# Optimization experiments

Measured on AMD Instinct MI355X. Metric: run time of the kernel, lower is better.

## Reference

```python
import jax, jax.numpy as jnp
import numpy as np

B, T, N = 32, 64, 2048
HID, HEADS, DH, BOT, MAX_LAG = 256, 8, 32, 64, 7


def setup_inputs() -> dict:
    key = jax.random.key(0)
    ks = jax.random.split(key, 12)
    def nrm(k, shape, s=0.05):
        return jax.random.normal(k, shape, jnp.float32) * s
    # delay logits init as in the module: log(softmaxed exp decay)
    w = np.exp(-np.arange(MAX_LAG + 1) / 3.0)
    w = w / w.sum()
    delay_logits = jnp.asarray(np.log(w + 1e-8), jnp.float32)
    # row-normalized adjacency prior (done in __init__ of the module)
    adj_raw = jax.random.uniform(ks[0], (N, N), jnp.float32)
    adj_prior = adj_raw / (adj_raw.sum(-1, keepdims=True) + 1e-8)
    return {
        "x": jax.random.normal(ks[1], (B, T, N), jnp.float32),
        "features": jax.random.normal(ks[2], (B, N, HID), jnp.float32),
        "delay_logits": delay_logits,
        "w_dp": nrm(ks[3], (1, HID)), "b_dp": jnp.zeros((HID,), jnp.float32),
        "w_qkv_low": nrm(ks[4], (HID, 3 * BOT)), "b_qkv_low": jnp.zeros((3 * BOT,), jnp.float32),
        "w_qkv_high": nrm(ks[5], (3 * BOT, 3 * HID)), "b_qkv_high": jnp.zeros((3 * HID,), jnp.float32),
        "w_out_low": nrm(ks[6], (HID, BOT)), "b_out_low": jnp.zeros((BOT,), jnp.float32),
        "w_out_high": nrm(ks[7], (BOT, HID)), "b_out_high": jnp.zeros((HID,), jnp.float32),
        "adj_prior": adj_prior,
        "geo_weight": jnp.array([0.3], jnp.float32),
        "ln_gamma": jnp.ones((HID,), jnp.float32),
        "ln_beta": jnp.zeros((HID,), jnp.float32),
    }


def reference(x, features, delay_logits, w_dp, b_dp,
              w_qkv_low, b_qkv_low, w_qkv_high, b_qkv_high,
              w_out_low, b_out_low, w_out_high, b_out_high,
              adj_prior, geo_weight, ln_gamma, ln_beta):
    # --- delay-weighted signal (generation interval) ---
    dw = jax.nn.softmax(delay_logits)                      # [max_lag+1]
    taus = min(MAX_LAG + 1, T)                              # static
    x_lags = jnp.flip(x, axis=1)[:, :taus]                  # [B,taus,N], lag tau = x[:, -(tau+1)]
    delayed = jnp.einsum('t,btn->bn', dw[:taus], x_lags)    # [B,N]
    delay_feat = delayed[:, :, None] * w_dp[0] + b_dp       # Linear(1, hidden)
    combined = features + 0.1 * delay_feat                  # [B,N,HID]

    # --- low-rank QKV ---
    qkv = (combined @ w_qkv_low + b_qkv_low) @ w_qkv_high + b_qkv_high  # [B,N,3*HID]
    q, k, v = jnp.split(qkv, 3, axis=-1)
    def to_heads(t):
        return t.reshape(B, N, HEADS, DH).transpose(0, 2, 1, 3)  # [B,H,N,dh]
    q, k, v = to_heads(q), to_heads(k), to_heads(v)

    # --- linear attention (elu+1 feature map, O(N)) ---
    qf = jax.nn.elu(q) + 1.0
    kf = jax.nn.elu(k) + 1.0
    kv = jnp.einsum('bhnd,bhne->bhde', kf, v)               # [B,H,dh,dh]
    k_sum = kf.sum(axis=2) + 1e-8                           # [B,H,dh]
    num = jnp.einsum('bhnd,bhde->bhne', qf, kv)             # [B,H,N,dh]
    den = jnp.einsum('bhnd,bhd->bhn', qf, k_sum)[..., None] + 1e-8
    attended = num / den

    # --- geo-adjacency blend ---
    gb = jax.nn.sigmoid(geo_weight[0])
    v_geo = jnp.einsum('nm,bhmd->bhnd', adj_prior, v)       # dense graph mixing
    attended = (1.0 - gb) * attended + gb * v_geo

    attended = attended.transpose(0, 2, 1, 3).reshape(B, N, HID)
    # dropout is identity in eval mode
    out = (attended @ w_out_low + b_out_low) @ w_out_high + b_out_high

    # --- residual + LayerNorm ---
    y = out + features
    mu = y.mean(-1, keepdims=True)
    var = ((y - mu) ** 2).mean(-1, keepdims=True)
    return (y - mu) / jnp.sqrt(var + 1e-5) * ln_gamma + ln_beta
```

## Files before the change

kernel.cpp:

```cpp
#include <hip/hip_runtime.h>
#include <hip/hip_bf16.h>
#include <stdint.h>

typedef unsigned short u16;
typedef float f4v __attribute__((ext_vector_type(4)));
typedef short s8v __attribute__((ext_vector_type(8)));


__device__ __forceinline__ float bf2f(u16 u) {
  union { float f; uint32_t i; } x; x.i = ((uint32_t)u) << 16; return x.f;
}
__device__ __forceinline__ u16 f2bf(float f) {
  uint32_t u = __float_as_uint(f);
  u = (u + 0x7FFFu + ((u >> 16) & 1u)) >> 16;
  return (u16)u;
}
__device__ __forceinline__ uint32_t pk2(float a, float b) {
  return (uint32_t)f2bf(a) | ((uint32_t)f2bf(b) << 16);
}
__device__ __forceinline__ void gload16(const void* g, void* l) {
  __builtin_amdgcn_global_load_lds((const __attribute__((address_space(1))) void*)g,
                                   (__attribute__((address_space(3))) void*)l, 16, 0, 0);
}

__global__ __launch_bounds__(256) void prep_all_k(
    const float* __restrict__ x, const float* __restrict__ dlog,
    const float* __restrict__ w_dp, const float* __restrict__ b_dp,
    const float* __restrict__ wql, const float* __restrict__ bql,
    const float* __restrict__ wqh, const float* __restrict__ wol,
    const float* __restrict__ bqh,
    float* __restrict__ wl_d, float* __restrict__ bl_p, float* __restrict__ delayed,
    u16* __restrict__ wqlT, u16* __restrict__ wqhT, u16* __restrict__ wvlT,
    float* __restrict__ cvl) {
  const int bid = blockIdx.x, t = threadIdx.x;
  if (bid < 256) {
    float mx = dlog[0];
#pragma unroll
    for (int i = 1; i < 8; ++i) mx = fmaxf(mx, dlog[i]);
    float w8[8], ssum = 0.f;
#pragma unroll
    for (int i = 0; i < 8; ++i) { w8[i] = __expf(dlog[i] - mx); ssum += w8[i]; }
    float inv = 1.f / ssum;
    int r = bid * 256 + t;
    int b = r >> 11, n = r & 2047;
    const float* xb = x + (size_t)b * 64 * 2048;
    float acc = 0.f;
#pragma unroll
    for (int tau = 0; tau < 8; ++tau) acc += w8[tau] * inv * xb[(size_t)(63 - tau) * 2048 + n];
    delayed[r] = acc;
  } else if (bid < 512) {
    int n = bid - 256;
    wqlT[(size_t)n * 256 + t] = f2bf(n < 192 ? wql[(size_t)t * 192 + n] : 0.f);
  } else if (bid < 1280) {
    int n = bid - 512;
    if (t < 192) wqhT[(size_t)n * 192 + t] = f2bf(wqh[(size_t)t * 768 + n]);
  } else if (bid < 1408) {
    int d = bid - 1280;
    __shared__ float wolc[256];
    if (d < 64) wolc[t] = wol[(size_t)t * 64 + d];
    __syncthreads();
    if (t < 192) {
      float s = 0.f;
      if (d < 64) {
        const float* wr = wqh + (size_t)t * 768 + 512;
        for (int c = 0; c < 256; ++c) s = fmaf(wr[c], wolc[c], s);
      }
      wvlT[(size_t)d * 192 + t] = f2bf(s);
    }
    if (t == 0 && d < 64) {
      float s = 0.f;
      for (int c = 0; c < 256; ++c) s = fmaf(bqh[512 + c], wolc[c], s);
      cvl[d] = s;
    }
  } else {
    if (t < 192) {
      float s1 = 0.f, s2 = 0.f;
      for (int k = 0; k < 256; ++k) {
        float w = wql[k * 192 + t];
        s1 += w_dp[k] * w;
        s2 += b_dp[k] * w;
      }
      wl_d[t] = 0.1f * s1;
      bl_p[t] = bql[t] + 0.1f * s2;
    }
  }
}

__global__ __launch_bounds__(256) void cvtadj_k(const float* __restrict__ in,
                                                u16* __restrict__ out) {
  size_t i = ((size_t)blockIdx.x * 256 + threadIdx.x) * 8;
  float4 a = *(const float4*)(in + i);
  float4 b = *(const float4*)(in + i + 4);
  uint4 q = {pk2(a.x, a.y), pk2(a.z, a.w), pk2(b.x, b.y), pk2(b.z, b.w)};
  *(uint4*)(out + i) = q;
}

struct MArgs {
  const u16* A;
  const float* Af32;
  const u16* adjb;
  const u16* Bt;
  const float* delayed; const float* wl_d; const float* bl_p;
  const float* bqh;
  const float* cvl;
  u16* low; u16* qf; u16* kf; u16* v; u16* vpt;
  u16* geopart;
};

enum { GLOW = 0, GQ = 1, GKV = 2, GGEO = 3, GVP = 4 };

template <int MODE>
__global__ __launch_bounds__(256) void mgemm_k(MArgs ma) {
  constexpr int KLOOP = (MODE == GLOW) ? 256 : (MODE == GGEO) ? 512 : 192;
  constexpr int LDA = (MODE == GLOW) ? 256 : (MODE == GGEO) ? 2048 : 192;
  constexpr int LDB = (MODE == GLOW) ? 256 : (MODE == GGEO) ? 2048 : 192;
  constexpr bool SWAPPED = (MODE == GLOW || MODE == GQ || MODE == GGEO);

  constexpr int SHN = (MODE == GKV) ? (128 * 136) : (128 * 128);
  __shared__ __align__(16) u16 SH[SHN];
  u16* Al = SH;
  u16* Bl = SH + 128 * 64;

  const int t = threadIdx.x;
  const int l = t & 63, w = t >> 6;
  const int wm = w >> 1, wn = w & 1;

  int ct, rt, bz = 0;
  if constexpr (MODE == GGEO) {
    int lin = blockIdx.x + 16 * blockIdx.y + 256 * blockIdx.z;
    int xcd = lin & 7, idx = lin >> 3;
    ct = idx & 15;
    int pid = xcd * 8 + (idx >> 4);
    rt = pid & 15;
    bz = pid >> 4;
  } else {
    constexpr int NCT = (MODE == GLOW || MODE == GQ) ? 2 : (MODE == GKV) ? 4 : 1;
    int lin = blockIdx.x + NCT * blockIdx.y;
    int xcd = lin & 7, idx = lin >> 3;
    ct = idx % NCT; rt = xcd * 64 + idx / NCT;
  }
  const int kbase = (MODE == GGEO) ? bz * 512 : 0;

  f4v acc[4][4] = {};

  for (int k0 = 0; k0 < KLOOP; k0 += 64) {
    __syncthreads();
#pragma unroll
    for (int s = 0; s < 4; ++s) {
      int c = s * 256 + t;
      int r = c >> 3, cc = c & 7;
      int g = ((cc & 3) ^ ((r >> 1) & 3)) | ((cc & 4) ^ ((r & 1) << 2));
      int row = rt * 128 + r;
      int kg = kbase + k0 + g * 8;
      if constexpr (MODE == GLOW) {
        const float* src = ma.Af32 + (size_t)row * LDA + kg;
        float4 x0 = *(const float4*)src;
        float4 x1 = *(const float4*)(src + 4);
        uint4 qq = {pk2(x0.x, x0.y), pk2(x0.z, x0.w), pk2(x1.x, x1.y), pk2(x1.z, x1.w)};
        *(uint4*)&Al[c * 8] = qq;
      } else if constexpr (MODE == GGEO) {
        gload16(ma.adjb + (size_t)row * 2048 + kg, (char*)Al + (s * 4 + w) * 1024);
      } else {
        gload16(ma.A + (size_t)row * LDA + kg, (char*)Al + (s * 4 + w) * 1024);
      }
      gload16(ma.Bt + (size_t)(ct * 128 + r) * LDB + kg,
              (char*)Bl + (s * 4 + w) * 1024);
    }
    __syncthreads();

#pragma unroll
    for (int kk = 0; kk < 64; kk += 32) {
      s8v fa[4], fb[4];
#pragma unroll
      for (int mr = 0; mr < 4; ++mr) {
        int ra = wm * 64 + mr * 16 + (l & 15);
        int ch = ((l >> 4) ^ ((ra >> 1) & 3)) | ((kk >> 3) ^ ((ra & 1) << 2));
        fa[mr] = *(const s8v*)(Al + ra * 64 + ch * 8);
      }
#pragma unroll
      for (int nr = 0; nr < 4; ++nr) {
        int rb = wn * 64 + nr * 16 + (l & 15);
        int cb = ((l >> 4) ^ ((rb >> 1) & 3)) | ((kk >> 3) ^ ((rb & 1) << 2));
        fb[nr] = *(const s8v*)(Bl + rb * 64 + cb * 8);
      }
      if constexpr (SWAPPED) {
#pragma unroll
        for (int mr = 0; mr < 4; ++mr)
#pragma unroll
          for (int nr = 0; nr < 4; ++nr)
            acc[mr][nr] = __builtin_amdgcn_mfma_f32_16x16x32_bf16(fb[nr], fa[mr], acc[mr][nr], 0, 0, 0);
      } else {
#pragma unroll
        for (int mr = 0; mr < 4; ++mr)
#pragma unroll
          for (int nr = 0; nr < 4; ++nr)
            acc[mr][nr] = __builtin_amdgcn_mfma_f32_16x16x32_bf16(fa[mr], fb[nr], acc[mr][nr], 0, 0, 0);
      }
    }
  }

  const int r0 = rt * 128 + wm * 64, c0 = ct * 128 + wn * 64;

  if constexpr (MODE == GVP) {
    const int lr = (l >> 4) * 4, lc = l & 15;
#pragma unroll
    for (int mr = 0; mr < 4; ++mr)
#pragma unroll
      for (int nr = 0; nr < 4; ++nr) {
        if (wn == 0) {
          int d = nr * 16 + lc;
          float cadd = ma.cvl[d];
          int n0 = (r0 + mr * 16 + lr) & 2047;
          int b = rt >> 4;
          ushort4 st = {f2bf(acc[mr][nr][0] + cadd), f2bf(acc[mr][nr][1] + cadd),
                        f2bf(acc[mr][nr][2] + cadd), f2bf(acc[mr][nr][3] + cadd)};
          *(ushort4*)(ma.vpt + ((size_t)(b * 64 + d)) * 2048 + n0) = st;
        }
      }
  } else if constexpr (MODE == GKV) {
    const int lr = (l >> 4) * 4, lc = l & 15;
    const bool isK = (ct < 2);
    __syncthreads();
#pragma unroll
    for (int nr = 0; nr < 4; ++nr) {
      int chat_l = wn * 64 + nr * 16 + lc;
      float bias = ma.bqh[256 + ct * 128 + chat_l];
#pragma unroll
      for (int mr = 0; mr < 4; ++mr) {
        int n_l = wm * 64 + mr * 16 + lr;
        float v0 = acc[mr][nr][0] + bias;
        float v1 = acc[mr][nr][1] + bias;
        float v2 = acc[mr][nr][2] + bias;
        float v3 = acc[mr][nr][3] + bias;
        if (isK) {
          v0 = (v0 > 0.f) ? (v0 + 1.f) : __expf(v0);
          v1 = (v1 > 0.f) ? (v1 + 1.f) : __expf(v1);
          v2 = (v2 > 0.f) ? (v2 + 1.f) : __expf(v2);
          v3 = (v3 > 0.f) ? (v3 + 1.f) : __expf(v3);
        }
        ushort4 st = {f2bf(v0), f2bf(v1), f2bf(v2), f2bf(v3)};
        *(ushort4*)&SH[chat_l * 136 + n_l] = st;
      }
    }
    __syncthreads();
    const int b = rt >> 4, nbase = (rt & 15) * 128;
#pragma unroll
    for (int s = 0; s < 8; ++s) {
      int idx = s * 256 + t;
      int chat_l = idx >> 4, nch = (idx & 15) * 8;
      uint4 q = *(const uint4*)&SH[chat_l * 136 + nch];
      int chat_g = ct * 128 + chat_l;
      u16* dst = isK ? (ma.kf + ((size_t)(b * 256 + chat_g)) * 2048)
                     : (ma.v + ((size_t)(b * 256 + chat_g - 256)) * 2048);
      *(uint4*)(dst + nbase + nch) = q;
    }
  } else {
    const int rowl = l & 15, colq = (l >> 4) * 4;
#pragma unroll
    for (int mr = 0; mr < 4; ++mr) {
      int row = r0 + mr * 16 + rowl;
#pragma unroll
      for (int nr = 0; nr < 4; ++nr) {
        int col0 = c0 + nr * 16 + colq;
        if constexpr (MODE == GLOW) {
          if (col0 < 192) {
            float dl = ma.delayed[row];
            float4 wd = *(const float4*)(ma.wl_d + col0);
            float4 bp = *(const float4*)(ma.bl_p + col0);
            ushort4 st = {f2bf(acc[mr][nr][0] + dl * wd.x + bp.x),
                          f2bf(acc[mr][nr][1] + dl * wd.y + bp.y),
                          f2bf(acc[mr][nr][2] + dl * wd.z + bp.z),
                          f2bf(acc[mr][nr][3] + dl * wd.w + bp.w)};
            *(ushort4*)(ma.low + (size_t)row * 192 + col0) = st;
          }
        } else if constexpr (MODE == GQ) {
          float4 bias = *(const float4*)(ma.bqh + col0);
          float v0 = acc[mr][nr][0] + bias.x;
          float v1 = acc[mr][nr][1] + bias.y;
          float v2 = acc[mr][nr][2] + bias.z;
          float v3 = acc[mr][nr][3] + bias.w;
          v0 = (v0 > 0.f) ? (v0 + 1.f) : __expf(v0);
          v1 = (v1 > 0.f) ? (v1 + 1.f) : __expf(v1);
          v2 = (v2 > 0.f) ? (v2 + 1.f) : __expf(v2);
          v3 = (v3 > 0.f) ? (v3 + 1.f) : __expf(v3);
          ushort4 st = {f2bf(v0), f2bf(v1), f2bf(v2), f2bf(v3)};
          *(ushort4*)(ma.qf + (size_t)row * 256 + col0) = st;
        } else {
          u16* dst = ma.geopart + (size_t)bz * 4194304;
          ushort4 st = {f2bf(acc[mr][nr][0]), f2bf(acc[mr][nr][1]),
                        f2bf(acc[mr][nr][2]), f2bf(acc[mr][nr][3])};
          *(ushort4*)(dst + (size_t)row * 2048 + col0) = st;
        }
      }
    }
  }
}

__global__ __launch_bounds__(256) void kvred_k(const u16* __restrict__ kfT,
                                               const u16* __restrict__ vT,
                                               float* __restrict__ kvpart,
                                               float* __restrict__ kspart) {
  const int z = blockIdx.x, h = blockIdx.y, b = blockIdx.z;
  const int t = threadIdx.x, l = t & 63, w = t >> 6;
  const size_t base = ((size_t)(b * 256 + h * 32)) * 2048 + z * 512 + w * 128;
  const u16* ka = kfT + base;
  const u16* vb = vT + base;
  f4v acc[2][2] = {};
  float ks[2] = {0.f, 0.f};
#pragma unroll
  for (int s = 0; s < 4; ++s) {
    int koff = s * 32 + (l >> 4) * 8;
    s8v fa[2], fb[2];
#pragma unroll
    for (int mr = 0; mr < 2; ++mr)
      fa[mr] = *(const s8v*)(ka + (size_t)(mr * 16 + (l & 15)) * 2048 + koff);
#pragma unroll
    for (int nr = 0; nr < 2; ++nr)
      fb[nr] = *(const s8v*)(vb + (size_t)(nr * 16 + (l & 15)) * 2048 + koff);
#pragma unroll
    for (int mr = 0; mr < 2; ++mr) {
      float sacc = 0.f;
#pragma unroll
      for (int j = 0; j < 8; ++j) sacc += bf2f((u16)fa[mr][j]);
      ks[mr] += sacc;
    }
#pragma unroll
    for (int mr = 0; mr < 2; ++mr)
#pragma unroll
      for (int nr = 0; nr < 2; ++nr)
        acc[mr][nr] = __builtin_amdgcn_mfma_f32_16x16x32_bf16(fa[mr], fb[nr], acc[mr][nr], 0, 0, 0);
  }
  ks[0] += __shfl_xor(ks[0], 16); ks[0] += __shfl_xor(ks[0], 32);
  ks[1] += __shfl_xor(ks[1], 16); ks[1] += __shfl_xor(ks[1], 32);

  __shared__ float kvs[4][32][32];
  __shared__ float kss[4][32];
#pragma unroll
  for (int mr = 0; mr < 2; ++mr)
#pragma unroll
    for (int nr = 0; nr < 2; ++nr)
#pragma unroll
      for (int i = 0; i < 4; ++i)
        kvs[w][mr * 16 + (l >> 4) * 4 + i][nr * 16 + (l & 15)] = acc[mr][nr][i];
  if (l < 16) { kss[w][l] = ks[0]; kss[w][16 + l] = ks[1]; }
  __syncthreads();
  float* kvp = kvpart + ((size_t)(z * 256 + b * 8 + h)) * 1024;
#pragma unroll
  for (int q = 0; q < 4; ++q) {
    int idx = q * 256 + t;
    kvp[idx] = kvs[0][idx >> 5][idx & 31] + kvs[1][idx >> 5][idx & 31] +
               kvs[2][idx >> 5][idx & 31] + kvs[3][idx >> 5][idx & 31];
  }
  if (t < 32)
    kspart[((size_t)(z * 256 + b * 8 + h)) * 32 + t] =
        kss[0][t] + kss[1][t] + kss[2][t] + kss[3][t];
}

__global__ __launch_bounds__(256) void gfin_k(const u16* __restrict__ qf,
                                              const float* __restrict__ rden,
                                              const u16* __restrict__ geopart,
                                              const u16* __restrict__ B2t,
                                              const float* __restrict__ cvec,
                                              const float* __restrict__ feats,
                                              const float* __restrict__ gamma,
                                              const float* __restrict__ beta,
                                              float* __restrict__ y) {
  __shared__ __align__(16) u16 Al[64 * 64];
  __shared__ __align__(16) u16 Bl[256 * 64];
  __shared__ float LN1[4][64], LN2[4][64];

  const int t = threadIdx.x;
  const int l = t & 63, w = t >> 6;
  const int rt = blockIdx.x;
  const int b = rt >> 5;

  f4v acc[4][4] = {};

  for (int k0 = 0; k0 < 320; k0 += 64) {
    __syncthreads();
#pragma unroll
    for (int s = 0; s < 2; ++s) {
      int c = s * 256 + t;
      int r = c >> 3, cc = c & 7;
      int g = ((cc & 3) ^ ((r >> 1) & 3)) | ((cc & 4) ^ ((r & 1) << 2));
      int row = rt * 64 + r;
      int kg = k0 + g * 8;
      if (k0 < 256) {
        float sc = rden[(size_t)row * 8 + (kg >> 5)];
        s8v qv = *(const s8v*)(qf + (size_t)row * 256 + kg);
        uint4 qq = {pk2(bf2f((u16)qv[0]) * sc, bf2f((u16)qv[1]) * sc),
                    pk2(bf2f((u16)qv[2]) * sc, bf2f((u16)qv[3]) * sc),
                    pk2(bf2f((u16)qv[4]) * sc, bf2f((u16)qv[5]) * sc),
                    pk2(bf2f((u16)qv[6]) * sc, bf2f((u16)qv[7]) * sc)};
        *(uint4*)&Al[c * 8] = qq;
      } else {
        int n = row & 2047;
        const u16* gp = geopart + (size_t)n * 2048 + b * 64 + (kg - 256);
        s8v p0 = *(const s8v*)(gp);
        s8v p1 = *(const s8v*)(gp + 4194304);
        s8v p2 = *(const s8v*)(gp + 8388608);
        s8v p3 = *(const s8v*)(gp + 12582912);
        float vv[8];
#pragma unroll
        for (int j = 0; j < 8; ++j)
          vv[j] = bf2f((u16)p0[j]) + bf2f((u16)p1[j]) + bf2f((u16)p2[j]) + bf2f((u16)p3[j]);
        uint4 qq = {pk2(vv[0], vv[1]), pk2(vv[2], vv[3]), pk2(vv[4], vv[5]), pk2(vv[6], vv[7])};
        *(uint4*)&Al[c * 8] = qq;
      }
    }
#pragma unroll
    for (int s = 0; s < 8; ++s) {
      int c = s * 256 + t;
      int r = c >> 3, cc = c & 7;
      int g = ((cc & 3) ^ ((r >> 1) & 3)) | ((cc & 4) ^ ((r & 1) << 2));
      gload16(B2t + ((size_t)b * 256 + r) * 320 + k0 + g * 8,
              (char*)Bl + (s * 4 + w) * 1024);
    }
    __syncthreads();

#pragma unroll
    for (int kk = 0; kk < 64; kk += 32) {
      s8v fa[4], fb[4];
#pragma unroll
      for (int mr = 0; mr < 4; ++mr) {
        int ra = mr * 16 + (l & 15);
        int ch = ((l >> 4) ^ ((ra >> 1) & 3)) | ((kk >> 3) ^ ((ra & 1) << 2));
        fa[mr] = *(const s8v*)(Al + ra * 64 + ch * 8);
      }
#pragma unroll
      for (int nr = 0; nr < 4; ++nr) {
        int rb = w * 64 + nr * 16 + (l & 15);
        int cb = ((l >> 4) ^ ((rb >> 1) & 3)) | ((kk >> 3) ^ ((rb & 1) << 2));
        fb[nr] = *(const s8v*)(Bl + rb * 64 + cb * 8);
      }
#pragma unroll
      for (int mr = 0; mr < 4; ++mr)
#pragma unroll
        for (int nr = 0; nr < 4; ++nr)
          acc[mr][nr] = __builtin_amdgcn_mfma_f32_16x16x32_bf16(fb[nr], fa[mr], acc[mr][nr], 0, 0, 0);
    }
  }

  const int rowl = l & 15, colq = (l >> 4) * 4;
  float s1v[4] = {0.f, 0.f, 0.f, 0.f}, s2v[4] = {0.f, 0.f, 0.f, 0.f};
#pragma unroll
  for (int mr = 0; mr < 4; ++mr) {
    int row = rt * 64 + mr * 16 + rowl;
#pragma unroll
    for (int nr = 0; nr < 4; ++nr) {
      int col0 = w * 64 + nr * 16 + colq;
      float4 cv = *(const float4*)(cvec + col0);
      float4 ft = *(const float4*)(feats + (size_t)row * 256 + col0);
      f4v vv = acc[mr][nr];
      vv[0] += cv.x + ft.x; vv[1] += cv.y + ft.y;
      vv[2] += cv.z + ft.z; vv[3] += cv.w + ft.w;
      acc[mr][nr] = vv;
      s1v[mr] += vv[0] + vv[1] + vv[2] + vv[3];
      s2v[mr] += vv[0] * vv[0] + vv[1] * vv[1] + vv[2] * vv[2] + vv[3] * vv[3];
    }
  }
#pragma unroll
  for (int mr = 0; mr < 4; ++mr) {
    s1v[mr] += __shfl_xor(s1v[mr], 16); s2v[mr] += __shfl_xor(s2v[mr], 16);
    s1v[mr] += __shfl_xor(s1v[mr], 32); s2v[mr] += __shfl_xor(s2v[mr], 32);
  }
  if (l < 16) {
#pragma unroll
    for (int mr = 0; mr < 4; ++mr) {
      LN1[w][mr * 16 + l] = s1v[mr];
      LN2[w][mr * 16 + l] = s2v[mr];
    }
  }
  __syncthreads();
#pragma unroll
  for (int mr = 0; mr < 4; ++mr) {
    int rl = mr * 16 + rowl;
    int row = rt * 64 + rl;
    float s1 = LN1[0][rl] + LN1[1][rl] + LN1[2][rl] + LN1[3][rl];
    float s2 = LN2[0][rl] + LN2[1][rl] + LN2[2][rl] + LN2[3][rl];
    float mu = s1 * (1.f / 256.f);
    float var = s2 * (1.f / 256.f) - mu * mu;
    float rstd = rsqrtf(fmaxf(var, 0.f) + 1e-5f);
#pragma unroll
    for (int nr = 0; nr < 4; ++nr) {
      int col0 = w * 64 + nr * 16 + colq;
      float4 g4 = *(const float4*)(gamma + col0);
      float4 b4 = *(const float4*)(beta + col0);
      f4v vv = acc[mr][nr];
      float4 o;
      o.x = (vv[0] - mu) * rstd * g4.x + b4.x;
      o.y = (vv[1] - mu) * rstd * g4.y + b4.y;
      o.z = (vv[2] - mu) * rstd * g4.z + b4.z;
      o.w = (vv[3] - mu) * rstd * g4.w + b4.w;
      *(float4*)(y + (size_t)row * 256 + col0) = o;
    }
  }
}

__global__ __launch_bounds__(64) void mmat_k(const float* __restrict__ kvpart,
                                             const float* __restrict__ wol,
                                             const float* __restrict__ geow,
                                             float* __restrict__ Mm) {
  const int bh = blockIdx.x;
  const int h = bh & 7, b = bh >> 3;
  const int c = threadIdx.x;
  __shared__ float kvs[32][32];
  for (int i = c; i < 1024; i += 64) {
    float s = 0.f;
#pragma unroll
    for (int p = 0; p < 4; ++p) s += kvpart[(size_t)(p * 256 + bh) * 1024 + i];
    kvs[i >> 5][i & 31] = s;
  }
  __syncthreads();
  float one_m = 1.f - 1.f / (1.f + __expf(-geow[0]));
  float acc[32];
#pragma unroll
  for (int d = 0; d < 32; ++d) acc[d] = 0.f;
  for (int e = 0; e < 32; ++e) {
    float w = wol[(size_t)(h * 32 + e) * 64 + c];
#pragma unroll
    for (int d = 0; d < 32; ++d) acc[d] = fmaf(kvs[d][e], w, acc[d]);
  }
  float* mp = Mm + (size_t)b * 16384 + (size_t)h * 32 * 64 + c;
#pragma unroll
  for (int d = 0; d < 32; ++d) mp[d * 64] = one_m * acc[d];
}

__global__ __launch_bounds__(256) void bprep_k(const float* __restrict__ Mm,
                                               const float* __restrict__ woh,
                                               const float* __restrict__ bol,
                                               const float* __restrict__ boh,
                                               const float* __restrict__ geow,
                                               u16* __restrict__ B2t,
                                               float* __restrict__ cvec) {
  const int kt = blockIdx.x, b = blockIdx.y;
  const int c = threadIdx.x;
  __shared__ float Ms[64][64];
#pragma unroll
  for (int i = 0; i < 16; ++i) {
    int flat = c + i * 256;
    int kk = flat >> 6, e = flat & 63;
    Ms[kk][e] = Mm[(size_t)b * 16384 + (size_t)(kt * 64 + kk) * 64 + e];
  }
  __syncthreads();
  float wcol[64];
#pragma unroll
  for (int e = 0; e < 64; ++e) wcol[e] = woh[(size_t)e * 256 + c];
  u16* dst = B2t + ((size_t)b * 256 + c) * 320;
  for (int kk = 0; kk < 64; ++kk) {
    float s = 0.f;
#pragma unroll
    for (int e = 0; e < 64; ++e) s = fmaf(Ms[kk][e], wcol[e], s);
    dst[kt * 64 + kk] = f2bf(s);
  }
  if (kt == 0) {
    float gb = 1.f / (1.f + __expf(-geow[0]));
#pragma unroll
    for (int d = 0; d < 64; ++d) dst[256 + d] = f2bf(gb * wcol[d]);
    if (b == 0) {
      float s = boh[c];
#pragma unroll
      for (int d = 0; d < 64; ++d) s = fmaf(bol[d], wcol[d], s);
      cvec[c] = s;
    }
  }
}

__global__ __launch_bounds__(256) void rden_k(const u16* __restrict__ qf,
                                              const float* __restrict__ kspart,
                                              float* __restrict__ rden) {
  const int t = threadIdx.x;
  const int b = (blockIdx.x * 16) >> 11;
  __shared__ float ksumf[256];
  {
    int h = t >> 5, e = t & 31;
    float s = 0.f;
#pragma unroll
    for (int p = 0; p < 4; ++p) s += kspart[(size_t)(p * 256 + b * 8 + h) * 32 + e];
    ksumf[t] = s + 1e-8f;
  }
  __syncthreads();
  const int row = blockIdx.x * 16 + (t >> 4);
  const int c0 = (t & 15) * 16;
  s8v q0 = *(const s8v*)(qf + (size_t)row * 256 + c0);
  s8v q1 = *(const s8v*)(qf + (size_t)row * 256 + c0 + 8);
  float part = 0.f;
#pragma unroll
  for (int j = 0; j < 8; ++j) part = fmaf(bf2f((u16)q0[j]), ksumf[c0 + j], part);
#pragma unroll
  for (int j = 0; j < 8; ++j) part = fmaf(bf2f((u16)q1[j]), ksumf[c0 + 8 + j], part);
  float den = part + __shfl_xor(part, 1);
  if ((t & 1) == 0) rden[(size_t)row * 8 + (c0 >> 5)] = 1.f / (den + 1e-8f);
}

extern "C" void kernel_launch(void* const* d_in, const int* in_sizes, int n_in,
                              void* d_out, int out_size, void* d_ws, size_t ws_size,
                              hipStream_t stream) {
  const float* x     = (const float*)d_in[0];
  const float* feats = (const float*)d_in[1];
  const float* dlog  = (const float*)d_in[2];
  const float* w_dp  = (const float*)d_in[3];
  const float* b_dp  = (const float*)d_in[4];
  const float* wql   = (const float*)d_in[5];
  const float* bql   = (const float*)d_in[6];
  const float* wqh   = (const float*)d_in[7];
  const float* bqh   = (const float*)d_in[8];
  const float* wol   = (const float*)d_in[9];
  const float* bol   = (const float*)d_in[10];
  const float* woh   = (const float*)d_in[11];
  const float* boh   = (const float*)d_in[12];
  const float* adj   = (const float*)d_in[13];
  const float* geow  = (const float*)d_in[14];
  const float* gamma = (const float*)d_in[15];
  const float* beta  = (const float*)d_in[16];

  char* ws = (char*)d_ws;
  constexpr size_t OFF_WLD   = 1024;
  constexpr size_t OFF_BLP   = 2048;
  constexpr size_t OFF_CVEC  = 4096;
  constexpr size_t OFF_CVL   = 5120;
  constexpr size_t OFF_DEL   = 8192;
  constexpr size_t OFF_WQLT  = 270336;
  constexpr size_t OFF_WQHT  = 401408;
  constexpr size_t OFF_WVLT  = 696320;
  constexpr size_t OFF_KSP   = 745472;
  constexpr size_t OFF_RDEN  = 876544;
  constexpr size_t OFF_MM    = 2973696;
  constexpr size_t OFF_B2T   = 5070848;
  constexpr size_t OFF_KVP   = OFF_B2T;
  constexpr size_t OFF_LOW   = 10444800;
  constexpr size_t OFF_QF    = 35610624;
  constexpr size_t OFF_KF    = 69165056;
  constexpr size_t OFF_VPT   = OFF_KF;
  constexpr size_t OFF_ADJB  = OFF_KF + 8388608;
  constexpr size_t OFF_V     = 102719488;
  constexpr size_t OFF_GPART = OFF_V;

  float* wl_d    = (float*)(ws + OFF_WLD);
  float* bl_p    = (float*)(ws + OFF_BLP);
  float* cvec    = (float*)(ws + OFF_CVEC);
  float* cvl     = (float*)(ws + OFF_CVL);
  float* delayed = (float*)(ws + OFF_DEL);
  float* kspart  = (float*)(ws + OFF_KSP);
  float* rden    = (float*)(ws + OFF_RDEN);
  float* Mm      = (float*)(ws + OFF_MM);
  float* kvpart  = (float*)(ws + OFF_KVP);
  u16* wqlT = (u16*)(ws + OFF_WQLT);
  u16* wqhT = (u16*)(ws + OFF_WQHT);
  u16* wvlT = (u16*)(ws + OFF_WVLT);
  u16* B2t  = (u16*)(ws + OFF_B2T);
  u16* adjb = (u16*)(ws + OFF_ADJB);

  MArgs ma{};
  ma.delayed = delayed; ma.wl_d = wl_d; ma.bl_p = bl_p; ma.bqh = bqh; ma.cvl = cvl;
  ma.adjb = adjb;
  ma.low = (u16*)(ws + OFF_LOW);
  ma.qf  = (u16*)(ws + OFF_QF);
  ma.kf  = (u16*)(ws + OFF_KF);
  ma.v   = (u16*)(ws + OFF_V);
  ma.vpt = (u16*)(ws + OFF_VPT);
  ma.geopart = (u16*)(ws + OFF_GPART);

  prep_all_k<<<1409, 256, 0, stream>>>(x, dlog, w_dp, b_dp, wql, bql, wqh, wol, bqh,
                                       wl_d, bl_p, delayed, wqlT, wqhT, wvlT, cvl);

  MArgs m0 = ma; m0.Af32 = feats; m0.Bt = wqlT;
  mgemm_k<GLOW><<<dim3(2, 512), 256, 0, stream>>>(m0);

  MArgs m1 = ma; m1.A = ma.low; m1.Bt = wqhT;
  mgemm_k<GQ><<<dim3(2, 512), 256, 0, stream>>>(m1);

  MArgs m1b = ma; m1b.A = ma.low; m1b.Bt = wqhT + (size_t)256 * 192;
  mgemm_k<GKV><<<dim3(4, 512), 256, 0, stream>>>(m1b);

  kvred_k<<<dim3(4, 8, 32), 256, 0, stream>>>(ma.kf, ma.v, kvpart, kspart);
  cvtadj_k<<<2048, 256, 0, stream>>>(adj, adjb);
  mmat_k<<<256, 64, 0, stream>>>(kvpart, wol, geow, Mm);
  rden_k<<<4096, 256, 0, stream>>>(ma.qf, kspart, rden);
  bprep_k<<<dim3(4, 32), 256, 0, stream>>>(Mm, woh, bol, boh, geow, B2t, cvec);

  MArgs m2 = ma; m2.A = ma.low; m2.Bt = wvlT;
  mgemm_k<GVP><<<dim3(1, 512), 256, 0, stream>>>(m2);

  MArgs m3 = ma; m3.Bt = ma.vpt;
  mgemm_k<GGEO><<<dim3(16, 16, 4), 256, 0, stream>>>(m3);

  gfin_k<<<1024, 256, 0, stream>>>(ma.qf, rden, ma.geopart, B2t, cvec,
                                   feats, gamma, beta, (float*)d_out);
  (void)in_sizes; (void)n_in; (void)out_size; (void)ws_size;
}
```

Baseline: 259.0 us.

## Fuse K/V projection GEMM with KV reduction to avoid materializing kf and v

Replaces the GKV GEMM mode plus the separate kvred kernel with one gkv kernel. Each block computes the K and V projections for one head over a 128-row tile, applies elu+1 to K, transposes the result through shared memory, and immediately forms partial kf^T v and k-sum products. This removes the global write and re-read of the full bf16 kf and v tensors. The cost is 16 partial slices per (batch, head) instead of 4, so mmat and rden now read more partial data, and the KV weight tiles are reloaded by each head block.

Result: faster. 247.3 us (-4.5%).

```diff
diff --git a/kernel.cpp b/kernel.cpp
--- a/kernel.cpp
+++ b/kernel.cpp
@@ -103,21 +103,20 @@
   const float* delayed; const float* wl_d; const float* bl_p;
   const float* bqh;
   const float* cvl;
-  u16* low; u16* qf; u16* kf; u16* v; u16* vpt;
+  u16* low; u16* qf; u16* vpt;
   u16* geopart;
 };
 
-enum { GLOW = 0, GQ = 1, GKV = 2, GGEO = 3, GVP = 4 };
+enum { GLOW = 0, GQ = 1, GGEO = 2, GVP = 3 };
 
 template <int MODE>
 __global__ __launch_bounds__(256) void mgemm_k(MArgs ma) {
   constexpr int KLOOP = (MODE == GLOW) ? 256 : (MODE == GGEO) ? 512 : 192;
   constexpr int LDA = (MODE == GLOW) ? 256 : (MODE == GGEO) ? 2048 : 192;
   constexpr int LDB = (MODE == GLOW) ? 256 : (MODE == GGEO) ? 2048 : 192;
-  constexpr bool SWAPPED = (MODE == GLOW || MODE == GQ || MODE == GGEO);
-
-  constexpr int SHN = (MODE == GKV) ? (128 * 136) : (128 * 128);
-  __shared__ __align__(16) u16 SH[SHN];
+  constexpr bool SWAPPED = (MODE != GVP);
+
+  __shared__ __align__(16) u16 SH[128 * 128];
   u16* Al = SH;
   u16* Bl = SH + 128 * 64;
 
@@ -134,7 +133,7 @@
     rt = pid & 15;
     bz = pid >> 4;
   } else {
-    constexpr int NCT = (MODE == GLOW || MODE == GQ) ? 2 : (MODE == GKV) ? 4 : 1;
+    constexpr int NCT = (MODE == GVP) ? 1 : 2;
     int lin = blockIdx.x + NCT * blockIdx.y;
     int xcd = lin & 7, idx = lin >> 3;
     ct = idx % NCT; rt = xcd * 64 + idx / NCT;
@@ -217,43 +216,6 @@
           *(ushort4*)(ma.vpt + ((size_t)(b * 64 + d)) * 2048 + n0) = st;
         }
       }
-  } else if constexpr (MODE == GKV) {
-    const int lr = (l >> 4) * 4, lc = l & 15;
-    const bool isK = (ct < 2);
-    __syncthreads();
-#pragma unroll
-    for (int nr = 0; nr < 4; ++nr) {
-      int chat_l = wn * 64 + nr * 16 + lc;
-      float bias = ma.bqh[256 + ct * 128 + chat_l];
-#pragma unroll
-      for (int mr = 0; mr < 4; ++mr) {
-        int n_l = wm * 64 + mr * 16 + lr;
-        float v0 = acc[mr][nr][0] + bias;
-        float v1 = acc[mr][nr][1] + bias;
-        float v2 = acc[mr][nr][2] + bias;
-        float v3 = acc[mr][nr][3] + bias;
-        if (isK) {
-          v0 = (v0 > 0.f) ? (v0 + 1.f) : __expf(v0);
-          v1 = (v1 > 0.f) ? (v1 + 1.f) : __expf(v1);
-          v2 = (v2 > 0.f) ? (v2 + 1.f) : __expf(v2);
-          v3 = (v3 > 0.f) ? (v3 + 1.f) : __expf(v3);
-        }
-        ushort4 st = {f2bf(v0), f2bf(v1), f2bf(v2), f2bf(v3)};
-        *(ushort4*)&SH[chat_l * 136 + n_l] = st;
-      }
-    }
-    __syncthreads();
-    const int b = rt >> 4, nbase = (rt & 15) * 128;
-#pragma unroll
-    for (int s = 0; s < 8; ++s) {
-      int idx = s * 256 + t;
-      int chat_l = idx >> 4, nch = (idx & 15) * 8;
-      uint4 q = *(const uint4*)&SH[chat_l * 136 + nch];
-      int chat_g = ct * 128 + chat_l;
-      u16* dst = isK ? (ma.kf + ((size_t)(b * 256 + chat_g)) * 2048)
-                     : (ma.v + ((size_t)(b * 256 + chat_g - 256)) * 2048);
-      *(uint4*)(dst + nbase + nch) = q;
-    }
   } else {
     const int rowl = l & 15, colq = (l >> 4) * 4;
 #pragma unroll
@@ -296,64 +258,145 @@
   }
 }
 
-__global__ __launch_bounds__(256) void kvred_k(const u16* __restrict__ kfT,
-                                               const u16* __restrict__ vT,
-                                               float* __restrict__ kvpart,
-                                               float* __restrict__ kspart) {
-  const int z = blockIdx.x, h = blockIdx.y, b = blockIdx.z;
-  const int t = threadIdx.x, l = t & 63, w = t >> 6;
-  const size_t base = ((size_t)(b * 256 + h * 32)) * 2048 + z * 512 + w * 128;
-  const u16* ka = kfT + base;
-  const u16* vb = vT + base;
-  f4v acc[2][2] = {};
+__global__ __launch_bounds__(256) void gkv_k(const u16* __restrict__ low,
+                                             const u16* __restrict__ wqhTkv,
+                                             const float* __restrict__ bqh,
+                                             float* __restrict__ kvpart,
+                                             float* __restrict__ kspart) {
+  __shared__ __align__(16) u16 SH[17152];
+  u16* Al = SH;
+  u16* Bl = SH + 128 * 64;
+  u16* T  = SH;
+  float* kvs = (float*)((char*)SH + 17408);
+  float* kss = (float*)((char*)SH + 17408 + 16384);
+
+  const int t = threadIdx.x;
+  const int l = t & 63, w = t >> 6;
+
+  int lin = blockIdx.x + 8 * blockIdx.y;
+  int xcd = lin & 7, idx = lin >> 3;
+  const int h = idx & 7;
+  const int rt = xcd * 64 + (idx >> 3);
+  const int b = rt >> 4, p = rt & 15;
+
+  f4v acc[2][4] = {};
+
+  for (int k0 = 0; k0 < 192; k0 += 64) {
+    __syncthreads();
+#pragma unroll
+    for (int s = 0; s < 4; ++s) {
+      int c = s * 256 + t;
+      int r = c >> 3, cc = c & 7;
+      int g = ((cc & 3) ^ ((r >> 1) & 3)) | ((cc & 4) ^ ((r & 1) << 2));
+      gload16(low + (size_t)(rt * 128 + r) * 192 + k0 + g * 8,
+              (char*)Al + (s * 4 + w) * 1024);
+    }
+#pragma unroll
+    for (int s = 0; s < 2; ++s) {
+      int c = s * 256 + t;
+      int r = c >> 3, cc = c & 7;
+      int g = ((cc & 3) ^ ((r >> 1) & 3)) | ((cc & 4) ^ ((r & 1) << 2));
+      int wqrow = (r < 32) ? (h * 32 + r) : (256 + h * 32 + (r - 32));
+      gload16(wqhTkv + (size_t)wqrow * 192 + k0 + g * 8,
+              (char*)Bl + (s * 4 + w) * 1024);
+    }
+    __syncthreads();
+
+#pragma unroll
+    for (int kk = 0; kk < 64; kk += 32) {
+      s8v fa[2], fb[4];
+#pragma unroll
+      for (int mr = 0; mr < 2; ++mr) {
+        int ra = w * 32 + mr * 16 + (l & 15);
+        int ch = ((l >> 4) ^ ((ra >> 1) & 3)) | ((kk >> 3) ^ ((ra & 1) << 2));
+        fa[mr] = *(const s8v*)(Al + ra * 64 + ch * 8);
+      }
+#pragma unroll
+      for (int nr = 0; nr < 4; ++nr) {
+        int rb = nr * 16 + (l & 15);
+        int cb = ((l >> 4) ^ ((rb >> 1) & 3)) | ((kk >> 3) ^ ((rb & 1) << 2));
+        fb[nr] = *(const s8v*)(Bl + rb * 64 + cb * 8);
+      }
+#pragma unroll
+      for (int mr = 0; mr < 2; ++mr)
+#pragma unroll
+        for (int nr = 0; nr < 4; ++nr)
+          acc[mr][nr] = __builtin_amdgcn_mfma_f32_16x16x32_bf16(fa[mr], fb[nr], acc[mr][nr], 0, 0, 0);
+    }
+  }
+
+  const int lr = (l >> 4) * 4, lc = l & 15;
+  __syncthreads();
+#pragma unroll
+  for (int nr = 0; nr < 4; ++nr) {
+    int cl = nr * 16 + lc;
+    float bias = (cl < 32) ? bqh[256 + h * 32 + cl] : bqh[512 + h * 32 + (cl - 32)];
+#pragma unroll
+    for (int mr = 0; mr < 2; ++mr) {
+      int n_l = w * 32 + mr * 16 + lr;
+      float v0 = acc[mr][nr][0] + bias;
+      float v1 = acc[mr][nr][1] + bias;
+      float v2 = acc[mr][nr][2] + bias;
+      float v3 = acc[mr][nr][3] + bias;
+      if (cl < 32) {
+        v0 = (v0 > 0.f) ? (v0 + 1.f) : __expf(v0);
+        v1 = (v1 > 0.f) ? (v1 + 1.f) : __expf(v1);
+        v2 = (v2 > 0.f) ? (v2 + 1.f) : __expf(v2);
+        v3 = (v3 > 0.f) ? (v3 + 1.f) : __expf(v3);
+      }
+      ushort4 st = {f2bf(v0), f2bf(v1), f2bf(v2), f2bf(v3)};
+      *(ushort4*)&T[cl * 136 + n_l] = st;
+    }
+  }
+  __syncthreads();
+
+  f4v acc2[2][2] = {};
   float ks[2] = {0.f, 0.f};
-#pragma unroll
-  for (int s = 0; s < 4; ++s) {
-    int koff = s * 32 + (l >> 4) * 8;
-    s8v fa[2], fb[2];
+  {
+    int koff = w * 32 + (l >> 4) * 8;
+    s8v fa2[2], fb2[2];
 #pragma unroll
     for (int mr = 0; mr < 2; ++mr)
-      fa[mr] = *(const s8v*)(ka + (size_t)(mr * 16 + (l & 15)) * 2048 + koff);
+      fa2[mr] = *(const s8v*)&T[(mr * 16 + (l & 15)) * 136 + koff];
 #pragma unroll
     for (int nr = 0; nr < 2; ++nr)
-      fb[nr] = *(const s8v*)(vb + (size_t)(nr * 16 + (l & 15)) * 2048 + koff);
+      fb2[nr] = *(const s8v*)&T[(32 + nr * 16 + (l & 15)) * 136 + koff];
 #pragma unroll
     for (int mr = 0; mr < 2; ++mr) {
       float sacc = 0.f;
 #pragma unroll
-      for (int j = 0; j < 8; ++j) sacc += bf2f((u16)fa[mr][j]);
-      ks[mr] += sacc;
+      for (int j = 0; j < 8; ++j) sacc += bf2f((u16)fa2[mr][j]);
+      ks[mr] = sacc;
     }
 #pragma unroll
     for (int mr = 0; mr < 2; ++mr)
 #pragma unroll
       for (int nr = 0; nr < 2; ++nr)
-        acc[mr][nr] = __builtin_amdgcn_mfma_f32_16x16x32_bf16(fa[mr], fb[nr], acc[mr][nr], 0, 0, 0);
+        acc2[mr][nr] = __builtin_amdgcn_mfma_f32_16x16x32_bf16(fa2[mr], fb2[nr], acc2[mr][nr], 0, 0, 0);
   }
   ks[0] += __shfl_xor(ks[0], 16); ks[0] += __shfl_xor(ks[0], 32);
   ks[1] += __shfl_xor(ks[1], 16); ks[1] += __shfl_xor(ks[1], 32);
 
-  __shared__ float kvs[4][32][32];
-  __shared__ float kss[4][32];
 #pragma unroll
   for (int mr = 0; mr < 2; ++mr)
 #pragma unroll
     for (int nr = 0; nr < 2; ++nr)
 #pragma unroll
       for (int i = 0; i < 4; ++i)
-        kvs[w][mr * 16 + (l >> 4) * 4 + i][nr * 16 + (l & 15)] = acc[mr][nr][i];
-  if (l < 16) { kss[w][l] = ks[0]; kss[w][16 + l] = ks[1]; }
+        kvs[(size_t)w * 1024 + (mr * 16 + (l >> 4) * 4 + i) * 32 + nr * 16 + (l & 15)] =
+            acc2[mr][nr][i];
+  if (l < 16) { kss[w * 32 + l] = ks[0]; kss[w * 32 + 16 + l] = ks[1]; }
   __syncthreads();
-  float* kvp = kvpart + ((size_t)(z * 256 + b * 8 + h)) * 1024;
+
+  float* kvp = kvpart + ((size_t)(p * 256 + b * 8 + h)) * 1024;
 #pragma unroll
   for (int q = 0; q < 4; ++q) {
     int idx = q * 256 + t;
-    kvp[idx] = kvs[0][idx >> 5][idx & 31] + kvs[1][idx >> 5][idx & 31] +
-               kvs[2][idx >> 5][idx & 31] + kvs[3][idx >> 5][idx & 31];
+    kvp[idx] = kvs[idx] + kvs[1024 + idx] + kvs[2048 + idx] + kvs[3072 + idx];
   }
   if (t < 32)
-    kspart[((size_t)(z * 256 + b * 8 + h)) * 32 + t] =
-        kss[0][t] + kss[1][t] + kss[2][t] + kss[3][t];
+    kspart[((size_t)(p * 256 + b * 8 + h)) * 32 + t] =
+        kss[t] + kss[32 + t] + kss[64 + t] + kss[96 + t];
 }
 
 __global__ __launch_bounds__(256) void gfin_k(const u16* __restrict__ qf,
@@ -508,7 +551,7 @@
   for (int i = c; i < 1024; i += 64) {
     float s = 0.f;
 #pragma unroll
-    for (int p = 0; p < 4; ++p) s += kvpart[(size_t)(p * 256 + bh) * 1024 + i];
+    for (int p = 0; p < 16; ++p) s += kvpart[(size_t)(p * 256 + bh) * 1024 + i];
     kvs[i >> 5][i & 31] = s;
   }
   __syncthreads();
@@ -576,7 +619,7 @@
     int h = t >> 5, e = t & 31;
     float s = 0.f;
 #pragma unroll
-    for (int p = 0; p < 4; ++p) s += kspart[(size_t)(p * 256 + b * 8 + h) * 32 + e];
+    for (int p = 0; p < 16; ++p) s += kspart[(size_t)(p * 256 + b * 8 + h) * 32 + e];
     ksumf[t] = s + 1e-8f;
   }
   __syncthreads();
@@ -623,17 +666,17 @@
   constexpr size_t OFF_WQLT  = 270336;
   constexpr size_t OFF_WQHT  = 401408;
   constexpr size_t OFF_WVLT  = 696320;
-  constexpr size_t OFF_KSP   = 745472;
   constexpr size_t OFF_RDEN  = 876544;
   constexpr size_t OFF_MM    = 2973696;
   constexpr size_t OFF_B2T   = 5070848;
-  constexpr size_t OFF_KVP   = OFF_B2T;
   constexpr size_t OFF_LOW   = 10444800;
   constexpr size_t OFF_QF    = 35610624;
   constexpr size_t OFF_KF    = 69165056;
   constexpr size_t OFF_VPT   = OFF_KF;
   constexpr size_t OFF_ADJB  = OFF_KF + 8388608;
   constexpr size_t OFF_V     = 102719488;
+  constexpr size_t OFF_KVP   = OFF_V;
+  constexpr size_t OFF_KSP   = OFF_V + 16777216;
   constexpr size_t OFF_GPART = OFF_V;
 
   float* wl_d    = (float*)(ws + OFF_WLD);
@@ -656,8 +699,6 @@
   ma.adjb = adjb;
   ma.low = (u16*)(ws + OFF_LOW);
   ma.qf  = (u16*)(ws + OFF_QF);
-  ma.kf  = (u16*)(ws + OFF_KF);
-  ma.v   = (u16*)(ws + OFF_V);
   ma.vpt = (u16*)(ws + OFF_VPT);
   ma.geopart = (u16*)(ws + OFF_GPART);
 
@@ -670,10 +711,9 @@
   MArgs m1 = ma; m1.A = ma.low; m1.Bt = wqhT;
   mgemm_k<GQ><<<dim3(2, 512), 256, 0, stream>>>(m1);
 
-  MArgs m1b = ma; m1b.A = ma.low; m1b.Bt = wqhT + (size_t)256 * 192;
-  mgemm_k<GKV><<<dim3(4, 512), 256, 0, stream>>>(m1b);
-
-  kvred_k<<<dim3(4, 8, 32), 256, 0, stream>>>(ma.kf, ma.v, kvpart, kspart);
+  gkv_k<<<dim3(8, 512), 256, 0, stream>>>(ma.low, wqhT + (size_t)256 * 192, bqh,
+                                          kvpart, kspart);
+
   cvtadj_k<<<2048, 256, 0, stream>>>(adj, adjb);
   mmat_k<<<256, 64, 0, stream>>>(kvpart, wol, geow, Mm);
   rden_k<<<4096, 256, 0, stream>>>(ma.qf, kspart, rden);
```
